# Optimization experiments

Measured on AMD Instinct MI355X. Metric: run time of the kernel, lower is better.

Reference implementation:

```python
import math
import jax, jax.numpy as jnp
import numpy as np

SCORE_THR = 0.05
NMS_THR = 0.5
MIN_SIZE = 0.01
MAX_DET = 100
SCALE_CLAMP = math.log(1000.0 / 16.0)
WX, WY, WW, WH = 10.0, 10.0, 5.0, 5.0  # BoxCoder weights


def setup_inputs() -> dict:
    key = jax.random.key(0)
    k1, k2, k3, k4 = jax.random.split(key, 4)
    B, N, C = 4, 2048, 3
    H = W = 800
    class_logits = 2.0 * jax.random.normal(k1, (B, N, C), dtype=jnp.float32)
    box_regression = 0.5 * jax.random.normal(k2, (B, N, 4 * C), dtype=jnp.float32)
    cxy = jax.random.uniform(k3, (B, N, 2), minval=0.0, maxval=float(W))
    wh = jax.random.uniform(k4, (B, N, 2), minval=4.0, maxval=100.0)
    proposals = jnp.concatenate([cxy - 0.5 * wh, cxy + 0.5 * wh], axis=-1)
    proposals = jnp.clip(proposals, 0.0, float(W))
    return {"class_logits": class_logits, "box_regression": box_regression,
            "proposals": proposals, "image_h": H, "image_w": W}


def _decode(rel, props):
    # rel: [N, C, 4] deltas, props: [N, 4] xyxy -> [N, C, 4] decoded boxes
    w = props[:, 2] - props[:, 0]
    h = props[:, 3] - props[:, 1]
    cx = props[:, 0] + 0.5 * w
    cy = props[:, 1] + 0.5 * h
    dx = rel[..., 0] / WX
    dy = rel[..., 1] / WY
    dw = jnp.minimum(rel[..., 2] / WW, SCALE_CLAMP)
    dh = jnp.minimum(rel[..., 3] / WH, SCALE_CLAMP)
    pcx = dx * w[:, None] + cx[:, None]
    pcy = dy * h[:, None] + cy[:, None]
    pw = jnp.exp(dw) * w[:, None]
    ph = jnp.exp(dh) * h[:, None]
    return jnp.stack([pcx - 0.5 * pw, pcy - 0.5 * ph,
                      pcx + 0.5 * pw, pcy + 0.5 * ph], axis=-1)


def _pairwise_iou(b):
    # b: [M, 4] -> [M, M]
    area = (b[:, 2] - b[:, 0]) * (b[:, 3] - b[:, 1])
    lt = jnp.maximum(b[:, None, :2], b[None, :, :2])
    rb = jnp.minimum(b[:, None, 2:], b[None, :, 2:])
    whd = jnp.clip(rb - lt, 0.0)
    inter = whd[..., 0] * whd[..., 1]
    return inter / (area[:, None] + area[None, :] - inter + 1e-7)


def _per_image(logits, rel, props, H, W):
    N, C = logits.shape
    scores = jax.nn.softmax(logits, axis=-1)               # [N, C]
    boxes = _decode(rel.reshape(N, C, 4), props)           # [N, C, 4]
    # clip to image (x in [0,W], y in [0,H])
    boxes = jnp.stack([jnp.clip(boxes[..., 0], 0.0, W),
                       jnp.clip(boxes[..., 1], 0.0, H),
                       jnp.clip(boxes[..., 2], 0.0, W),
                       jnp.clip(boxes[..., 3], 0.0, H)], axis=-1)
    # drop background class and flatten -> M = N*(C-1)
    boxes = boxes[:, 1:, :].reshape(-1, 4)
    scores = scores[:, 1:].reshape(-1)
    labels = jnp.broadcast_to(jnp.arange(1, C), (N, C - 1)).reshape(-1)
    valid = ((scores > SCORE_THR)
             & (boxes[:, 2] - boxes[:, 0] >= MIN_SIZE)
             & (boxes[:, 3] - boxes[:, 1] >= MIN_SIZE))
    # batched_nms via per-class coordinate offset
    offset = labels.astype(boxes.dtype) * (jnp.max(boxes) + 1.0)
    ob = boxes + offset[:, None]
    sort_key = jnp.where(valid, scores, -jnp.inf)
    order = jnp.argsort(-sort_key)
    bs, ss, ls, vs, obs = boxes[order], scores[order], labels[order], valid[order], ob[order]
    iou = _pairwise_iou(obs)                               # [M, M]
    M = bs.shape[0]
    idxs = jnp.arange(M)
    def body(i, keep):
        sup = keep[i] & (iou[i] > NMS_THR) & (idxs > i)
        return keep & ~sup
    keep = jax.lax.fori_loop(0, M, body, vs)
    sel = jnp.argsort(~keep, stable=True)[:MAX_DET]        # kept first, score order preserved
    kb, ksc, kl, kk = bs[sel], ss[sel], ls[sel], keep[sel]
    kb = jnp.where(kk[:, None], kb, 0.0)
    ksc = jnp.where(kk, ksc, 0.0)
    kl = jnp.where(kk, kl, 0)
    return kb, ksc, kl, kk


def reference(class_logits, box_regression, proposals, image_h, image_w):
    H = jnp.float32(image_h)
    W = jnp.float32(image_w)
    f = jax.vmap(lambda l, r, p: _per_image(l, r, p, H, W))
    boxes, scores, labels, keep = f(class_logits, box_regression, proposals)
    return boxes, scores, labels, keep
```

## Files before the change

kernel.cpp:

```cpp
#include <hip/hip_runtime.h>
#include <stdint.h>

#define BB 4
#define NN 2048
#define CC 3
#define MM (NN * (CC - 1))
#define MAXDET 100
#define SCORE_THR 0.05f
#define NMS_THR 0.5f
#define MIN_SIZE 0.01f
#define TTARGET 256
#define SSKCAP 1024
#define TILE 128

#define SCORE_OFF (BB * MAXDET * 4)
#define LABEL_OFF (SCORE_OFF + BB * MAXDET)
#define KEEP_OFF (LABEL_OFF + BB * MAXDET)
#define STASH(b, j) (SCORE_OFF + (b) * MAXDET + 96 + (j))

__device__ __forceinline__ void wave_lds_sync() {
  __builtin_amdgcn_wave_barrier();
  __builtin_amdgcn_s_waitcnt(0xC07F);
  __builtin_amdgcn_wave_barrier();
}

__device__ __forceinline__ bool iou_gt(const float4 A, const float aA,
                                       const float4 B, const float aB) {
#pragma clang fp contract(off)
  float ltx = fmaxf(A.x, B.x), lty = fmaxf(A.y, B.y);
  float rbx = fminf(A.z, B.z), rby = fminf(A.w, B.w);
  float iw = fmaxf(rbx - ltx, 0.0f), ih = fmaxf(rby - lty, 0.0f);
  float inter = iw * ih;
  float denom = ((aA + aB) - inter) + 1e-7f;
  return inter / denom > NMS_THR;
}

__global__ __launch_bounds__(512) void decode_kernel(const float* __restrict__ logits,
                                                     const float* __restrict__ rel,
                                                     const float* __restrict__ props,
                                                     const int* __restrict__ ph,
                                                     const int* __restrict__ pw,
                                                     float4* __restrict__ cand_box,
                                                     unsigned long long* __restrict__ keys,
                                                     unsigned* __restrict__ hist_g,
                                                     float* __restrict__ out) {
#pragma clang fp contract(off)
  __shared__ float red[512];
  __shared__ unsigned lhist[1024];
  int tid = threadIdx.x;
  int t = blockIdx.x * 512 + tid;
  int b = t >> 11;
  int n = t & 2047;
  float Hf = (float)ph[0];
  float Wf = (float)pw[0];

  lhist[tid] = 0u;
  lhist[tid + 512] = 0u;
  __syncthreads();

  const float* lg = logits + (size_t)t * CC;
  float l0 = lg[0], l1 = lg[1], l2 = lg[2];
  float mx = fmaxf(l0, fmaxf(l1, l2));
  float e0 = expf(l0 - mx), e1 = expf(l1 - mx), e2 = expf(l2 - mx);
  float ssum = (e0 + e1) + e2;

  float4 pr = ((const float4*)props)[t];
  float w = pr.z - pr.x, h = pr.w - pr.y;
  float cx = pr.x + 0.5f * w, cy = pr.y + 0.5f * h;
  const float4* rl = (const float4*)(rel + (size_t)t * 12);
  const float SCALE_CLAMP = 4.135166556742356f;

  float lmax = 0.0f;
  for (int c = 1; c < CC; ++c) {
    float4 rv = rl[c];
    float score = (c == 1 ? e1 : e2) / ssum;
    float dx = rv.x / 10.0f;
    float dy = rv.y / 10.0f;
    float dw = fminf(rv.z / 5.0f, SCALE_CLAMP);
    float dh = fminf(rv.w / 5.0f, SCALE_CLAMP);
    float pcx = dx * w + cx;
    float pcy = dy * h + cy;
    float bw = expf(dw) * w;
    float bh = expf(dh) * h;
    float x1 = pcx - 0.5f * bw, y1 = pcy - 0.5f * bh;
    float x2 = pcx + 0.5f * bw, y2 = pcy + 0.5f * bh;
    x1 = fminf(fmaxf(x1, 0.0f), Wf);
    y1 = fminf(fmaxf(y1, 0.0f), Hf);
    x2 = fminf(fmaxf(x2, 0.0f), Wf);
    y2 = fminf(fmaxf(y2, 0.0f), Hf);

    lmax = fmaxf(lmax, fmaxf(fmaxf(x1, y1), fmaxf(x2, y2)));

    bool valid = (score > SCORE_THR) && (x2 - x1 >= MIN_SIZE) && (y2 - y1 >= MIN_SIZE);
    int m = n * (CC - 1) + (c - 1);
    cand_box[(size_t)b * MM + m] = make_float4(x1, y1, x2, y2);
    unsigned long long key = 0ull;
    if (valid) {
      unsigned sb = __float_as_uint(score);
      key = (((unsigned long long)sb) << 32) |
            (unsigned long long)(0xFFFFFFFFu - (unsigned)m);
      atomicAdd(&lhist[(sb >> 16) & 1023], 1u);
    }
    keys[(size_t)b * MM + m] = key;
  }

  red[tid] = lmax;
  __syncthreads();
  for (int s2 = 256; s2 > 0; s2 >>= 1) {
    if (tid < s2) red[tid] = fmaxf(red[tid], red[tid + s2]);
    __syncthreads();
  }
  if (tid == 0) out[STASH(b, blockIdx.x & 3)] = red[0];

  hist_g[blockIdx.x * 1024 + tid] = lhist[tid];
  hist_g[blockIdx.x * 1024 + tid + 512] = lhist[tid + 512];
}

__device__ void bitonic_sort_desc(unsigned long long* a, int P, int tid) {
  int prev_big = 1;
  for (int size = 2; size <= P; size <<= 1) {
    for (int stride = size >> 1; stride > 0; stride >>= 1) {
      int big = (stride >= 128);
      if (big | prev_big) __syncthreads(); else wave_lds_sync();
      for (int i = tid; i < (P >> 1); i += 512) {
        int lo = 2 * i - (i & (stride - 1));
        int hi = lo + stride;
        bool asc = ((lo & size) != 0);
        unsigned long long x = a[lo], y = a[hi];
        if ((x > y) == asc) { a[lo] = y; a[hi] = x; }
      }
      prev_big = big;
    }
  }
  __syncthreads();
}

__device__ void bitonic_sort_desc_reg512(unsigned long long* a,
                                         unsigned long long* xbuf0,
                                         unsigned long long* xbuf1,
                                         int T, int tid) {
  unsigned long long v = (tid < T) ? a[tid] : 0ull;
  int xb = 0;
  for (int size = 2; size <= 512; size <<= 1) {
    for (int stride = size >> 1; stride > 0; stride >>= 1) {
      unsigned long long o;
      if (stride < 64) {
        o = __shfl_xor(v, stride);
      } else {
        unsigned long long* buf = xb ? xbuf1 : xbuf0;
        __syncthreads();
        buf[tid] = v;
        __syncthreads();
        o = buf[tid ^ stride];
        xb ^= 1;
      }
      bool is_lo = (tid & stride) == 0;
      bool asc = (tid & size) != 0;
      bool take_min = (asc == is_lo);
      bool o_less = (o < v);
      unsigned long long mn = o_less ? o : v;
      unsigned long long mx = o_less ? v : o;
      v = take_min ? mn : mx;
    }
  }
  __syncthreads();
  a[tid] = v;
  __syncthreads();
}

__device__ int tiled_nms(const unsigned long long* keys_s, int count,
                         const float4* __restrict__ cbg, float off_base,
                         const float4* sboxall, const unsigned short* map, int use_map,
                         float4* tob, float4* trb, float* tarea,
                         ulonglong2* smask, int* sflag, int* knew,
                         float4* kept_ob, float4* kept_raw, float* kept_area,
                         unsigned long long* kept_key, int* s_nnew, int tid) {
#pragma clang fp contract(off)
  int wv = tid >> 6, lane = tid & 63;
  int cnt = 0;
  for (int base = 0; base < count && cnt < MAXDET; base += TILE) {
    int tsz = (count - base < TILE) ? (count - base) : TILE;
    if (tid < tsz) {
      unsigned long long key = keys_s[base + tid];
      int m = (int)(0xFFFFFFFFu - (unsigned)key);
      float4 bx = use_map ? sboxall[map[m]] : cbg[m];
      int lbl = (m & 1) + 1;
      float off = (float)lbl * off_base;
      float4 ob = make_float4(bx.x + off, bx.y + off, bx.z + off, bx.w + off);
      tob[tid] = ob;
      trb[tid] = bx;
      tarea[tid] = (ob.z - ob.x) * (ob.w - ob.y);
    }
    __syncthreads();

    float4 bi0 = tob[lane];
    float ai0 = tarea[lane];
    float4 bi1 = tob[lane + 64];
    float ai1 = tarea[lane + 64];
    float4 kb0 = kept_ob[(lane < cnt) ? lane : 0];
    float ka0 = kept_area[(lane < cnt) ? lane : 0];
    float4 kb1 = kept_ob[(lane + 64 < cnt) ? lane + 64 : 0];
    float ka1 = kept_area[(lane + 64 < cnt) ? lane + 64 : 0];

    for (int j = wv; j < tsz; j += 8) {
      float4 aj = tob[j];
      float aaj = tarea[j];
      unsigned long long w0 = 0ull, w1 = 0ull;
      if (j < 63) {
        bool p = (lane > j) && (lane < tsz) && iou_gt(aj, aaj, bi0, ai0);
        w0 = __ballot(p);
      }
      if (j < 127) {
        int i = lane + 64;
        bool p = (i > j) && (i < tsz) && iou_gt(aj, aaj, bi1, ai1);
        w1 = __ballot(p);
      }
      bool s = false;
      if (cnt > 0) {
        if (lane < cnt && iou_gt(kb0, ka0, aj, aaj)) s = true;
        if (cnt > 64 && lane + 64 < cnt && iou_gt(kb1, ka1, aj, aaj)) s = true;
      }
      int anyk = __any(s);
      if (lane == 0) {
        smask[j].x = w0;
        smask[j].y = w1;
        sflag[j] = anyk;
      }
    }
    __syncthreads();

    if (tid < 64) {
      bool f0 = (lane < tsz) && (sflag[lane] != 0);
      unsigned long long remv0 = __ballot(f0);
      bool f1 = (lane + 64 < tsz) && (sflag[lane + 64] != 0);
      unsigned long long remv1 = __ballot(f1);
      ulonglong2 pre[4];
#pragma unroll
      for (int k = 0; k < 4; ++k) pre[k] = smask[(k < tsz) ? k : 0];
      int c = cnt, nk = 0;
      for (int j = 0; j < tsz; ++j) {
        ulonglong2 row = pre[j & 3];
        int nxt = j + 4;
        pre[j & 3] = smask[(nxt < tsz) ? nxt : 0];
        bool rem = (j < 64) ? (((remv0 >> j) & 1ull) != 0ull)
                            : (((remv1 >> (j - 64)) & 1ull) != 0ull);
        if (!rem) {
          if (lane == 0) knew[nk] = j;
          nk++;
          c++;
          remv0 |= row.x;
          remv1 |= row.y;
          if (c >= MAXDET) break;
        }
      }
      if (lane == 0) *s_nnew = nk;
    }
    __syncthreads();

    int nnew = *s_nnew;
    if (tid < nnew) {
      int j = knew[tid];
      kept_ob[cnt + tid] = tob[j];
      kept_raw[cnt + tid] = trb[j];
      kept_area[cnt + tid] = tarea[j];
      kept_key[cnt + tid] = keys_s[base + j];
    }
    cnt += nnew;
    __syncthreads();
  }
  return cnt;
}

__global__ __launch_bounds__(512) void nms_kernel(const float4* __restrict__ cand_box,
                                                  const unsigned long long* __restrict__ keys,
                                                  const unsigned* __restrict__ hist_g,
                                                  float* __restrict__ out) {
#pragma clang fp contract(off)
  __shared__ __align__(16) unsigned long long sk[MM];
  __shared__ __align__(16) unsigned long long ssk[SSKCAP];
  __shared__ __align__(16) float4 sbox[SSKCAP];
  __shared__ unsigned short map[MM];
  __shared__ __align__(16) float4 tob[TILE];
  __shared__ __align__(16) float4 trb[TILE];
  __shared__ float tarea[TILE];
  __shared__ __align__(16) ulonglong2 smask[TILE];
  __shared__ int sflag[TILE];
  __shared__ int knew[TILE];
  __shared__ float4 kept_ob[MAXDET];
  __shared__ float4 kept_raw[MAXDET];
  __shared__ float kept_area[MAXDET];
  __shared__ unsigned long long kept_key[MAXDET];
  __shared__ int s_scnt, s_thr, s_vtot, s_cnt, s_fb, s_nnew;

  int b = blockIdx.x;
  int tid = threadIdx.x;
  int lane = tid & 63;
  const float4* cbg = cand_box + (size_t)b * MM;

  const ulonglong2* kg = (const ulonglong2*)(keys + (size_t)b * MM);
  ulonglong2 kr[4];
#pragma unroll
  for (int j = 0; j < 4; ++j) kr[j] = kg[j * 512 + tid];

  if (tid == 0) { s_scnt = 0; s_fb = 0; s_cnt = 0; }
  float m01 = fmaxf(out[STASH(b, 0)], out[STASH(b, 1)]);
  float m23 = fmaxf(out[STASH(b, 2)], out[STASH(b, 3)]);
  float off_base = fmaxf(m01, m23) + 1.0f;

  if (tid < 64) {
    const unsigned* hg = hist_g + (b * 4) * 1024 + tid * 16;
    unsigned own[16];
#pragma unroll
    for (int i = 0; i < 16; ++i)
      own[i] = hg[i] + hg[1024 + i] + hg[2048 + i] + hg[3072 + i];
    unsigned psum = 0;
#pragma unroll
    for (int i = 0; i < 16; ++i) psum += own[i];
    unsigned s = psum;
    for (int d = 1; d < 64; d <<= 1) {
      unsigned o = __shfl_down(s, d);
      if (tid + d < 64) s += o;
    }
    unsigned after = s - psum;
    int best = -1;
    unsigned run = after;
#pragma unroll
    for (int i = 15; i >= 0; --i) {
      run += own[i];
      if (best < 0 && run >= TTARGET) best = tid * 16 + i;
    }
    int gb = best;
    for (int d = 1; d < 64; d <<= 1) {
      int o = __shfl_down(gb, d);
      if (tid + d < 64) gb = (o > gb) ? o : gb;
    }
    if (tid == 0) {
      s_thr = (gb < 0) ? 0 : gb;
      s_vtot = (int)s;
    }
  }
  __syncthreads();
  int thr = s_thr;
  int Vtot = s_vtot;

#pragma unroll
  for (int j = 0; j < 4; ++j) {
    int m0 = 1024 * j + 2 * tid;
    float4 b0 = cbg[m0];
    float4 b1 = cbg[m0 + 1];
#pragma unroll
    for (int half = 0; half < 2; ++half) {
      unsigned long long key = half ? kr[j].y : kr[j].x;
      unsigned hik = (unsigned)(key >> 32);
      bool pred = (hik != 0u) && ((int)((hik >> 16) & 1023) >= thr);
      unsigned long long mask = __ballot(pred);
      int ofs = __popcll(mask & ((1ull << lane) - 1ull));
      int basea = 0;
      if (lane == 0 && mask) basea = atomicAdd(&s_scnt, (int)__popcll(mask));
      basea = __shfl(basea, 0);
      if (pred) {
        int pos = basea + ofs;
        if (pos < SSKCAP) {
          ssk[pos] = key;
          sbox[pos] = half ? b1 : b0;
          map[m0 + half] = (unsigned short)pos;
        }
      }
    }
  }
  __syncthreads();
  int T = s_scnt;

  if (T <= SSKCAP) {
    if (T <= 512) {
      bitonic_sort_desc_reg512(ssk, sk, sk + 512, T, tid);
    } else {
      int P = 1;
      while (P < T) P <<= 1;
      for (int i = T + tid; i < P; i += 512) ssk[i] = 0ull;
      __syncthreads();
      bitonic_sort_desc(ssk, P, tid);
    }
    int cnt = tiled_nms(ssk, T, cbg, off_base, sbox, map, 1, tob, trb, tarea,
                        smask, sflag, knew, kept_ob, kept_raw, kept_area,
                        kept_key, &s_nnew, tid);
    if (tid == 0) {
      s_cnt = cnt;
      s_fb = (cnt < MAXDET && T < Vtot) ? 1 : 0;
    }
  } else {
    if (tid == 0) s_fb = 1;
  }
  __syncthreads();

  if (s_fb) {
    ulonglong2* skp = (ulonglong2*)sk;
#pragma unroll
    for (int j = 0; j < 4; ++j) skp[j * 512 + tid] = kr[j];
    __syncthreads();
    bitonic_sort_desc(sk, MM, tid);
    int cnt = tiled_nms(sk, Vtot, cbg, off_base, sbox, map, 0, tob, trb, tarea,
                        smask, sflag, knew, kept_ob, kept_raw, kept_area,
                        kept_key, &s_nnew, tid);
    if (tid == 0) s_cnt = cnt;
    __syncthreads();
  }

  int cnt = s_cnt;
  if (tid < MAXDET) {
    float4 bx = make_float4(0.0f, 0.0f, 0.0f, 0.0f);
    float sc = 0.0f, lb = 0.0f, kp = 0.0f;
    if (tid < cnt) {
      unsigned long long key = kept_key[tid];
      int m = (int)(0xFFFFFFFFu - (unsigned)key);
      bx = kept_raw[tid];
      sc = __uint_as_float((unsigned)(key >> 32));
      lb = (float)((m & 1) + 1);
      kp = 1.0f;
    }
    float* obp = out + (size_t)b * MAXDET * 4 + (size_t)tid * 4;
    obp[0] = bx.x; obp[1] = bx.y; obp[2] = bx.z; obp[3] = bx.w;
    out[SCORE_OFF + b * MAXDET + tid] = sc;
    out[LABEL_OFF + b * MAXDET + tid] = lb;
    out[KEEP_OFF + b * MAXDET + tid] = kp;
  }
}

extern "C" void kernel_launch(void* const* d_in, const int* in_sizes, int n_in,
                              void* d_out, int out_size, void* d_ws, size_t ws_size,
                              hipStream_t stream) {
  const float* logits = (const float*)d_in[0];
  const float* rel = (const float*)d_in[1];
  const float* props = (const float*)d_in[2];
  const int* ph = (const int*)d_in[3];
  const int* pw = (const int*)d_in[4];
  float* out = (float*)d_out;

  char* ws = (char*)d_ws;
  float4* cand_box = (float4*)ws;
  unsigned long long* keys = (unsigned long long*)(ws + (size_t)BB * MM * 16);
  unsigned* hist_g = (unsigned*)(ws + (size_t)BB * MM * 16 + (size_t)BB * MM * 8);

  decode_kernel<<<16, 512, 0, stream>>>(logits, rel, props, ph, pw, cand_box,
                                        keys, hist_g, out);
  nms_kernel<<<BB, 512, 0, stream>>>(cand_box, keys, hist_g, out);
}
```

Baseline: 94.72 us.

## Fuse decode and NMS into one per-image kernel with boxes in LDS

Merges the decode kernel into the NMS kernel, so each of the four blocks decodes its own image's 2048 proposals directly into shared memory and builds the score histogram and max-coordinate reduction locally. This removes the second launch and the global workspace round-trip for boxes, keys and histograms. Keeping all 4096 boxes in LDS also drops the compacted box copy and index map. The cost is that decode now runs on only 4 blocks instead of 16, and LDS use per block grows (64KB of boxes plus the key arrays), which could limit occupancy.

```diff
diff --git a/kernel.cpp b/kernel.cpp
--- a/kernel.cpp
+++ b/kernel.cpp
@@ -16,7 +16,6 @@
 #define SCORE_OFF (BB * MAXDET * 4)
 #define LABEL_OFF (SCORE_OFF + BB * MAXDET)
 #define KEEP_OFF (LABEL_OFF + BB * MAXDET)
-#define STASH(b, j) (SCORE_OFF + (b) * MAXDET + 96 + (j))
 
 __device__ __forceinline__ void wave_lds_sync() {
   __builtin_amdgcn_wave_barrier();
@@ -33,87 +32,6 @@
   float inter = iw * ih;
   float denom = ((aA + aB) - inter) + 1e-7f;
   return inter / denom > NMS_THR;
-}
-
-__global__ __launch_bounds__(512) void decode_kernel(const float* __restrict__ logits,
-                                                     const float* __restrict__ rel,
-                                                     const float* __restrict__ props,
-                                                     const int* __restrict__ ph,
-                                                     const int* __restrict__ pw,
-                                                     float4* __restrict__ cand_box,
-                                                     unsigned long long* __restrict__ keys,
-                                                     unsigned* __restrict__ hist_g,
-                                                     float* __restrict__ out) {
-#pragma clang fp contract(off)
-  __shared__ float red[512];
-  __shared__ unsigned lhist[1024];
-  int tid = threadIdx.x;
-  int t = blockIdx.x * 512 + tid;
-  int b = t >> 11;
-  int n = t & 2047;
-  float Hf = (float)ph[0];
-  float Wf = (float)pw[0];
-
-  lhist[tid] = 0u;
-  lhist[tid + 512] = 0u;
-  __syncthreads();
-
-  const float* lg = logits + (size_t)t * CC;
-  float l0 = lg[0], l1 = lg[1], l2 = lg[2];
-  float mx = fmaxf(l0, fmaxf(l1, l2));
-  float e0 = expf(l0 - mx), e1 = expf(l1 - mx), e2 = expf(l2 - mx);
-  float ssum = (e0 + e1) + e2;
-
-  float4 pr = ((const float4*)props)[t];
-  float w = pr.z - pr.x, h = pr.w - pr.y;
-  float cx = pr.x + 0.5f * w, cy = pr.y + 0.5f * h;
-  const float4* rl = (const float4*)(rel + (size_t)t * 12);
-  const float SCALE_CLAMP = 4.135166556742356f;
-
-  float lmax = 0.0f;
-  for (int c = 1; c < CC; ++c) {
-    float4 rv = rl[c];
-    float score = (c == 1 ? e1 : e2) / ssum;
-    float dx = rv.x / 10.0f;
-    float dy = rv.y / 10.0f;
-    float dw = fminf(rv.z / 5.0f, SCALE_CLAMP);
-    float dh = fminf(rv.w / 5.0f, SCALE_CLAMP);
-    float pcx = dx * w + cx;
-    float pcy = dy * h + cy;
-    float bw = expf(dw) * w;
-    float bh = expf(dh) * h;
-    float x1 = pcx - 0.5f * bw, y1 = pcy - 0.5f * bh;
-    float x2 = pcx + 0.5f * bw, y2 = pcy + 0.5f * bh;
-    x1 = fminf(fmaxf(x1, 0.0f), Wf);
-    y1 = fminf(fmaxf(y1, 0.0f), Hf);
-    x2 = fminf(fmaxf(x2, 0.0f), Wf);
-    y2 = fminf(fmaxf(y2, 0.0f), Hf);
-
-    lmax = fmaxf(lmax, fmaxf(fmaxf(x1, y1), fmaxf(x2, y2)));
-
-    bool valid = (score > SCORE_THR) && (x2 - x1 >= MIN_SIZE) && (y2 - y1 >= MIN_SIZE);
-    int m = n * (CC - 1) + (c - 1);
-    cand_box[(size_t)b * MM + m] = make_float4(x1, y1, x2, y2);
-    unsigned long long key = 0ull;
-    if (valid) {
-      unsigned sb = __float_as_uint(score);
-      key = (((unsigned long long)sb) << 32) |
-            (unsigned long long)(0xFFFFFFFFu - (unsigned)m);
-      atomicAdd(&lhist[(sb >> 16) & 1023], 1u);
-    }
-    keys[(size_t)b * MM + m] = key;
-  }
-
-  red[tid] = lmax;
-  __syncthreads();
-  for (int s2 = 256; s2 > 0; s2 >>= 1) {
-    if (tid < s2) red[tid] = fmaxf(red[tid], red[tid + s2]);
-    __syncthreads();
-  }
-  if (tid == 0) out[STASH(b, blockIdx.x & 3)] = red[0];
-
-  hist_g[blockIdx.x * 1024 + tid] = lhist[tid];
-  hist_g[blockIdx.x * 1024 + tid + 512] = lhist[tid + 512];
 }
 
 __device__ void bitonic_sort_desc(unsigned long long* a, int P, int tid) {
@@ -169,11 +87,10 @@
 }
 
 __device__ int tiled_nms(const unsigned long long* keys_s, int count,
-                         const float4* __restrict__ cbg, float off_base,
-                         const float4* sboxall, const unsigned short* map, int use_map,
-                         float4* tob, float4* trb, float* tarea,
+                         const float4* sboxes, float off_base,
+                         float4* tob, float* tarea,
                          ulonglong2* smask, int* sflag, int* knew,
-                         float4* kept_ob, float4* kept_raw, float* kept_area,
+                         float4* kept_ob, float* kept_area,
                          unsigned long long* kept_key, int* s_nnew, int tid) {
 #pragma clang fp contract(off)
   int wv = tid >> 6, lane = tid & 63;
@@ -183,12 +100,11 @@
     if (tid < tsz) {
       unsigned long long key = keys_s[base + tid];
       int m = (int)(0xFFFFFFFFu - (unsigned)key);
-      float4 bx = use_map ? sboxall[map[m]] : cbg[m];
+      float4 bx = sboxes[m];
       int lbl = (m & 1) + 1;
       float off = (float)lbl * off_base;
       float4 ob = make_float4(bx.x + off, bx.y + off, bx.z + off, bx.w + off);
       tob[tid] = ob;
-      trb[tid] = bx;
       tarea[tid] = (ob.z - ob.x) * (ob.w - ob.y);
     }
     __syncthreads();
@@ -261,7 +177,6 @@
     if (tid < nnew) {
       int j = knew[tid];
       kept_ob[cnt + tid] = tob[j];
-      kept_raw[cnt + tid] = trb[j];
       kept_area[cnt + tid] = tarea[j];
       kept_key[cnt + tid] = keys_s[base + j];
     }
@@ -271,23 +186,24 @@
   return cnt;
 }
 
-__global__ __launch_bounds__(512) void nms_kernel(const float4* __restrict__ cand_box,
-                                                  const unsigned long long* __restrict__ keys,
-                                                  const unsigned* __restrict__ hist_g,
-                                                  float* __restrict__ out) {
+__global__ __launch_bounds__(512) void fused_kernel(const float* __restrict__ logits,
+                                                    const float* __restrict__ rel,
+                                                    const float* __restrict__ props,
+                                                    const int* __restrict__ ph,
+                                                    const int* __restrict__ pw,
+                                                    float* __restrict__ out) {
 #pragma clang fp contract(off)
+  __shared__ __align__(16) float4 sboxes[MM];
   __shared__ __align__(16) unsigned long long sk[MM];
   __shared__ __align__(16) unsigned long long ssk[SSKCAP];
-  __shared__ __align__(16) float4 sbox[SSKCAP];
-  __shared__ unsigned short map[MM];
+  __shared__ unsigned hist[1024];
+  __shared__ float red[512];
   __shared__ __align__(16) float4 tob[TILE];
-  __shared__ __align__(16) float4 trb[TILE];
   __shared__ float tarea[TILE];
   __shared__ __align__(16) ulonglong2 smask[TILE];
   __shared__ int sflag[TILE];
   __shared__ int knew[TILE];
   __shared__ float4 kept_ob[MAXDET];
-  __shared__ float4 kept_raw[MAXDET];
   __shared__ float kept_area[MAXDET];
   __shared__ unsigned long long kept_key[MAXDET];
   __shared__ int s_scnt, s_thr, s_vtot, s_cnt, s_fb, s_nnew;
@@ -295,24 +211,81 @@
   int b = blockIdx.x;
   int tid = threadIdx.x;
   int lane = tid & 63;
-  const float4* cbg = cand_box + (size_t)b * MM;
-
-  const ulonglong2* kg = (const ulonglong2*)(keys + (size_t)b * MM);
+
+  hist[tid] = 0u;
+  hist[tid + 512] = 0u;
+  if (tid == 0) { s_scnt = 0; s_fb = 0; s_cnt = 0; }
+  __syncthreads();
+
+  float Hf = (float)ph[0];
+  float Wf = (float)pw[0];
+  const float SCALE_CLAMP = 4.135166556742356f;
   ulonglong2 kr[4];
-#pragma unroll
-  for (int j = 0; j < 4; ++j) kr[j] = kg[j * 512 + tid];
-
-  if (tid == 0) { s_scnt = 0; s_fb = 0; s_cnt = 0; }
-  float m01 = fmaxf(out[STASH(b, 0)], out[STASH(b, 1)]);
-  float m23 = fmaxf(out[STASH(b, 2)], out[STASH(b, 3)]);
-  float off_base = fmaxf(m01, m23) + 1.0f;
+  float lmax = 0.0f;
+#pragma unroll
+  for (int k = 0; k < 4; ++k) {
+    int n = tid + k * 512;
+    int t = b * NN + n;
+    const float* lg = logits + (size_t)t * CC;
+    float l0 = lg[0], l1 = lg[1], l2 = lg[2];
+    float mx = fmaxf(l0, fmaxf(l1, l2));
+    float e0 = expf(l0 - mx), e1 = expf(l1 - mx), e2 = expf(l2 - mx);
+    float ssum = (e0 + e1) + e2;
+
+    float4 pr = ((const float4*)props)[t];
+    float w = pr.z - pr.x, h = pr.w - pr.y;
+    float cx = pr.x + 0.5f * w, cy = pr.y + 0.5f * h;
+    const float4* rl = (const float4*)(rel + (size_t)t * 12);
+
+    unsigned long long kk[2];
+    for (int c = 1; c < CC; ++c) {
+      float4 rv = rl[c];
+      float score = (c == 1 ? e1 : e2) / ssum;
+      float dx = rv.x / 10.0f;
+      float dy = rv.y / 10.0f;
+      float dw = fminf(rv.z / 5.0f, SCALE_CLAMP);
+      float dh = fminf(rv.w / 5.0f, SCALE_CLAMP);
+      float pcx = dx * w + cx;
+      float pcy = dy * h + cy;
+      float bw = expf(dw) * w;
+      float bh = expf(dh) * h;
+      float x1 = pcx - 0.5f * bw, y1 = pcy - 0.5f * bh;
+      float x2 = pcx + 0.5f * bw, y2 = pcy + 0.5f * bh;
+      x1 = fminf(fmaxf(x1, 0.0f), Wf);
+      y1 = fminf(fmaxf(y1, 0.0f), Hf);
+      x2 = fminf(fmaxf(x2, 0.0f), Wf);
+      y2 = fminf(fmaxf(y2, 0.0f), Hf);
+
+      lmax = fmaxf(lmax, fmaxf(fmaxf(x1, y1), fmaxf(x2, y2)));
+
+      bool valid = (score > SCORE_THR) && (x2 - x1 >= MIN_SIZE) && (y2 - y1 >= MIN_SIZE);
+      int m = n * (CC - 1) + (c - 1);
+      sboxes[m] = make_float4(x1, y1, x2, y2);
+      unsigned long long key = 0ull;
+      if (valid) {
+        unsigned sb = __float_as_uint(score);
+        key = (((unsigned long long)sb) << 32) |
+              (unsigned long long)(0xFFFFFFFFu - (unsigned)m);
+        atomicAdd(&hist[(sb >> 16) & 1023], 1u);
+      }
+      kk[c - 1] = key;
+    }
+    kr[k].x = kk[0];
+    kr[k].y = kk[1];
+  }
+
+  red[tid] = lmax;
+  __syncthreads();
+  for (int s2 = 256; s2 > 0; s2 >>= 1) {
+    if (tid < s2) red[tid] = fmaxf(red[tid], red[tid + s2]);
+    __syncthreads();
+  }
+  float off_base = red[0] + 1.0f;
 
   if (tid < 64) {
-    const unsigned* hg = hist_g + (b * 4) * 1024 + tid * 16;
     unsigned own[16];
 #pragma unroll
-    for (int i = 0; i < 16; ++i)
-      own[i] = hg[i] + hg[1024 + i] + hg[2048 + i] + hg[3072 + i];
+    for (int i = 0; i < 16; ++i) own[i] = hist[tid * 16 + i];
     unsigned psum = 0;
 #pragma unroll
     for (int i = 0; i < 16; ++i) psum += own[i];
@@ -345,9 +318,6 @@
 
 #pragma unroll
   for (int j = 0; j < 4; ++j) {
-    int m0 = 1024 * j + 2 * tid;
-    float4 b0 = cbg[m0];
-    float4 b1 = cbg[m0 + 1];
 #pragma unroll
     for (int half = 0; half < 2; ++half) {
       unsigned long long key = half ? kr[j].y : kr[j].x;
@@ -360,11 +330,7 @@
       basea = __shfl(basea, 0);
       if (pred) {
         int pos = basea + ofs;
-        if (pos < SSKCAP) {
-          ssk[pos] = key;
-          sbox[pos] = half ? b1 : b0;
-          map[m0 + half] = (unsigned short)pos;
-        }
+        if (pos < SSKCAP) ssk[pos] = key;
       }
     }
   }
@@ -381,9 +347,8 @@
       __syncthreads();
       bitonic_sort_desc(ssk, P, tid);
     }
-    int cnt = tiled_nms(ssk, T, cbg, off_base, sbox, map, 1, tob, trb, tarea,
-                        smask, sflag, knew, kept_ob, kept_raw, kept_area,
-                        kept_key, &s_nnew, tid);
+    int cnt = tiled_nms(ssk, T, sboxes, off_base, tob, tarea, smask, sflag,
+                        knew, kept_ob, kept_area, kept_key, &s_nnew, tid);
     if (tid == 0) {
       s_cnt = cnt;
       s_fb = (cnt < MAXDET && T < Vtot) ? 1 : 0;
@@ -399,9 +364,8 @@
     for (int j = 0; j < 4; ++j) skp[j * 512 + tid] = kr[j];
     __syncthreads();
     bitonic_sort_desc(sk, MM, tid);
-    int cnt = tiled_nms(sk, Vtot, cbg, off_base, sbox, map, 0, tob, trb, tarea,
-                        smask, sflag, knew, kept_ob, kept_raw, kept_area,
-                        kept_key, &s_nnew, tid);
+    int cnt = tiled_nms(sk, Vtot, sboxes, off_base, tob, tarea, smask, sflag,
+                        knew, kept_ob, kept_area, kept_key, &s_nnew, tid);
     if (tid == 0) s_cnt = cnt;
     __syncthreads();
   }
@@ -413,7 +377,7 @@
     if (tid < cnt) {
       unsigned long long key = kept_key[tid];
       int m = (int)(0xFFFFFFFFu - (unsigned)key);
-      bx = kept_raw[tid];
+      bx = sboxes[m];
       sc = __uint_as_float((unsigned)(key >> 32));
       lb = (float)((m & 1) + 1);
       kp = 1.0f;
@@ -435,13 +399,7 @@
   const int* ph = (const int*)d_in[3];
   const int* pw = (const int*)d_in[4];
   float* out = (float*)d_out;
-
-  char* ws = (char*)d_ws;
-  float4* cand_box = (float4*)ws;
-  unsigned long long* keys = (unsigned long long*)(ws + (size_t)BB * MM * 16);
-  unsigned* hist_g = (unsigned*)(ws + (size_t)BB * MM * 16 + (size_t)BB * MM * 8);
-
-  decode_kernel<<<16, 512, 0, stream>>>(logits, rel, props, ph, pw, cand_box,
-                                        keys, hist_g, out);
-  nms_kernel<<<BB, 512, 0, stream>>>(cand_box, keys, hist_g, out);
-}
+  (void)d_ws; (void)ws_size;
+
+  fused_kernel<<<BB, 512, 0, stream>>>(logits, rel, props, ph, pw, out);
+}
```

New measurement: 93.28 us. Within noise of the previous version (-1.5%).
